# Performance work log

Hardware: AMD Instinct MI355X
Metric: run time of the kernel (lower is better)

The kernel has to match this reference:

```python
import jax, jax.numpy as jnp
from jax import lax
import numpy as np

# Module hyperparameters (match init_kwargs)
N = 4            # number of multiplex cells per feature map
NUM_FM = 64      # feature maps in the input
NF = N * NUM_FM  # lateral channel count = 256
H = W = 32       # feature map height/width
D = 2            # lateral neighborhood radius
PRD = 2          # padding repair distance (must equal D for symmetric pad)
KS = 2 * D + 1   # lateral kernel size = 5
IOTA = 0.1       # blend of activation vs lateral support for winner selection
B = 16           # batch size


def minmax_fm(x):
    """Min-max normalize each feature map (over the last two dims) to [0,1].
    Degenerate (constant) maps map to 0."""
    mn = jnp.min(x, axis=(-2, -1), keepdims=True)
    mx = jnp.max(x, axis=(-2, -1), keepdims=True)
    denom = mx - mn
    safe = jnp.where(denom > 0, denom, 1.0)
    return jnp.where(denom > 0, (x - mn) / safe, 0.0)


def _pad(A):
    # pad_activations: zeros of shape (.., PRD+D+H, PRD+D+W), A at [PRD:-PRD]
    # with PRD == D this is symmetric (PRD, D) padding.
    return jnp.pad(A, ((0, 0), (0, 0), (PRD, D), (PRD, D)))


def _conv(x, w):
    # x: (B, Cin, H', W'), w: (Cout, Cin, KS, KS) -> VALID conv (padding=0)
    return lax.conv_general_dilated(x, w, (1, 1), 'VALID',
                                    dimension_numbers=('NCHW', 'OIHW', 'NCHW'))


def setup_inputs() -> dict:
    key = jax.random.key(0)
    k1, k2 = jax.random.split(key)
    A = jax.random.uniform(k1, (B, NUM_FM, H, W), dtype=jnp.float32)
    K = jax.random.normal(k2, (NF, NF, KS, KS), dtype=jnp.float32)  # trained lateral kernel
    S = jnp.ones((NF,), dtype=jnp.float32)                          # scaling param
    return {"A": A, "K": K, "S": S}


def reference(A, K, S):
    batch = A.shape[0]
    # A.repeat(1, n, 1, 1): tile input n times along channels -> (B, NF, H, W)
    A_rep = jnp.tile(A, (1, N, 1, 1))

    # First lateral pass: conv with minmax-normalized K^T, scaled by S, minmaxed.
    L1 = _conv(_pad(A_rep), minmax_fm(jnp.swapaxes(K, 0, 1))) / NUM_FM
    L1 = L1 * S[None, :, None, None]
    L1 = minmax_fm(L1)

    # Winner-take-all multiplex selection (deterministic branch):
    s = jnp.sum((1.0 - IOTA) * A_rep + IOTA * L1, axis=(-2, -1))  # (B, NF)
    s = jnp.swapaxes(s.reshape(batch, N, NUM_FM), 1, 2)            # (B, NUM_FM, N)
    A_max = jnp.argmax(s, axis=-1)                                  # (B, NUM_FM)
    fm_idx = NUM_FM * A_max + jnp.arange(NUM_FM)                    # (B, NUM_FM) channel ids

    # Active-channel mask (complement = inactive_multiplex_idx in the original)
    active = jnp.zeros((batch, NF), dtype=bool)
    active = active.at[jnp.arange(batch)[:, None], fm_idx].set(True)

    # Zero inactive channels of A (tmp_A) and diagonal K[i,i] for inactive i
    # (large_K[b, idx, idx] = 0 is pairwise/diagonal fancy indexing in torch).
    tmp_A = A_rep * active[:, :, None, None].astype(A_rep.dtype)
    eye = jnp.eye(NF, dtype=bool)
    kill = eye[None, :, :] & (~active)[:, :, None]                  # (B, NF, NF)
    large_K = jnp.where(kill[..., None, None], 0.0, K[None])        # (B, NF, NF, KS, KS)

    # Second lateral pass: per-sample conv with per-sample kernel.
    pA = _pad(tmp_A)

    def per_sample(x, Kb):
        w = minmax_fm(jnp.swapaxes(Kb, 0, 1))
        return _conv(x[None], w)[0]

    L2 = jax.vmap(per_sample)(pA, large_K) / NUM_FM                 # (B, NF, H, W)

    # Gather winning channels: filtered_L (B, NUM_FM, H, W)
    return jnp.take_along_axis(L2, fm_idx[:, :, None, None], axis=1)
```

## Files before the change

kernel.cpp:

```cpp
#include <hip/hip_runtime.h>


#define NFM 64
#define NMX 4
#define NFC 256
#define HW 1024
#define KK 25

typedef unsigned short u16;
typedef short short8 __attribute__((ext_vector_type(8)));
typedef float f32x4 __attribute__((ext_vector_type(4)));

__device__ __forceinline__ u16 f2bfbits(float f) {
    unsigned int u = __float_as_uint(f);
    u += 0x7fffu + ((u >> 16) & 1u);
    return (u16)(u >> 16);
}
__device__ __forceinline__ float bf2f(u16 v) {
    return __uint_as_float(((unsigned int)v) << 16);
}

__global__ __launch_bounds__(256) void kprep(const float* __restrict__ K,
                                             float* __restrict__ wsum2) {
    __shared__ __align__(16) float buf[64 * KK];
    int g = blockIdx.x & 63, o0 = (blockIdx.x >> 6) * 64;
    int t = threadIdx.x;
    float wacc[KK];
#pragma unroll
    for (int k = 0; k < KK; ++k) wacc[k] = 0.f;

    for (int n = 0; n < NMX; ++n) {
        int i = n * NFM + g;
        const float4* src = (const float4*)(K + (i * NFC + o0) * KK);
        __syncthreads();
        ((float4*)buf)[t] = src[t];
        if (t < 144) ((float4*)buf)[t + 256] = src[t + 256];
        __syncthreads();
        if (t < 64) {
            float v[KK];
            float mn = 1e30f, mx = -1e30f;
#pragma unroll
            for (int k = 0; k < KK; ++k) {
                v[k] = buf[t * KK + k];
                mn = fminf(mn, v[k]);
                mx = fmaxf(mx, v[k]);
            }
            float d = mx - mn;
            float r = d > 0.f ? 1.f / d : 0.f;
#pragma unroll
            for (int k = 0; k < KK; ++k) wacc[k] += (v[k] - mn) * r;
        }
    }
    __syncthreads();
    if (t < 64) {
#pragma unroll
        for (int k = 0; k < KK; ++k) buf[t * KK + k] = wacc[k];
    }
    __syncthreads();
    float4* dst = (float4*)(wsum2 + (g * NFC + o0) * KK);
    dst[t] = ((float4*)buf)[t];
    if (t < 144) dst[t + 256] = ((float4*)buf)[t + 256];
}

__global__ __launch_bounds__(256) void kpackW(const float* __restrict__ wsum2,
                                              char* __restrict__ Wpk) {
    int id = blockIdx.x * 256 + threadIdx.x;
    int o = id / 200;
    int rem = id - o * 200;
    int ks = rem >> 2, quad = rem & 3;
    int dydx = ks >> 1;
    int gb = (ks & 1) * 32 + quad * 8;
    short8 hs, ls;
#pragma unroll
    for (int j = 0; j < 8; ++j) {
        float v = wsum2[((gb + j) * NFC + o) * KK + dydx];
        u16 h = f2bfbits(v);
        float lo = v - bf2f(h);
        hs[j] = (short)h;
        ls[j] = (short)f2bfbits(lo);
    }
    char* base = Wpk + (((o >> 4) * 50 + ks) * 2048) + (quad * 16 + (o & 15)) * 16;
    *(short8*)(base) = hs;
    *(short8*)(base + 1024) = ls;
}

__global__ __launch_bounds__(512, 4) void kscore(const float* __restrict__ A,
                                                 const char* __restrict__ Wpk,
                                                 float4* __restrict__ part) {
    __shared__ u16 slabh[6 * 36 * 72];
    __shared__ u16 slabl[6 * 36 * 72];
    int t = threadIdx.x;
    int mh = blockIdx.x, yb2 = blockIdx.y, b = blockIdx.z;
    int y0 = yb2 * 2;
    int lane = t & 63;
    int wv = __builtin_amdgcn_readfirstlane(t >> 6);
    int n15 = lane & 15, quad = lane >> 4;

    const float* Ab = A + b * NFM * HW;
    for (int ry = 0; ry < 6; ++ry) {
        int gy = y0 - 2 + ry;
        bool rowok = (gy >= 0) && (gy < 32);
        for (int c = 0; c < 5; ++c) {
            int id2 = c * 512 + t;
            if (id2 < 2304) {
                int g = (id2 * 3641) >> 17;
                int xi = id2 - g * 36;
                float v = 0.f;
                if (rowok && xi >= 2 && xi < 34)
                    v = Ab[g * HW + gy * 32 + xi - 2];
                u16 h = f2bfbits(v);
                u16 l = f2bfbits(v - bf2f(h));
                int idx = (ry * 36 + xi) * 72 + g;
                slabh[idx] = h;
                slabl[idx] = l;
            }
        }
    }
    __syncthreads();

    f32x4 acc[4];
#pragma unroll
    for (int p = 0; p < 4; ++p)
#pragma unroll
        for (int r = 0; r < 4; ++r) acc[p][r] = 0.f;

    const char* wbase = Wpk + ((mh * 8 + wv) * 50) * 2048 + lane * 16;
    short8 cah = *(const short8*)(wbase);
    short8 cal = *(const short8*)(wbase + 1024);

    for (int ks = 0; ks < 50; ++ks) {
        int ksn = ks < 49 ? ks + 1 : 49;
        const char* nb = wbase + (ksn << 11);
        short8 nah = *(const short8*)nb;
        short8 nal = *(const short8*)(nb + 1024);

        int dydx = ks >> 1;
        int gh = (ks & 1) * 32;
        int dy = dydx / 5, dx = dydx - dy * 5;
        short8 bh[4], bl[4];
#pragma unroll
        for (int p = 0; p < 4; ++p) {
            int r = p >> 1, nt = p & 1;
            int addr = ((r + dy) * 36 + nt * 16 + n15 + dx) * 72 + gh + quad * 8;
            bh[p] = *(const short8*)(slabh + addr);
            bl[p] = *(const short8*)(slabl + addr);
        }
#pragma unroll
        for (int p = 0; p < 4; ++p) {
            acc[p] = __builtin_amdgcn_mfma_f32_16x16x32_bf16(cah, bh[p], acc[p], 0, 0, 0);
            acc[p] = __builtin_amdgcn_mfma_f32_16x16x32_bf16(cah, bl[p], acc[p], 0, 0, 0);
            acc[p] = __builtin_amdgcn_mfma_f32_16x16x32_bf16(cal, bh[p], acc[p], 0, 0, 0);
        }
        cah = nah;
        cal = nal;
    }

#pragma unroll
    for (int reg = 0; reg < 4; ++reg) {
        float v0 = acc[0][reg], v1 = acc[1][reg];
        float v2 = acc[2][reg], v3 = acc[3][reg];
        float mn = fminf(fminf(v0, v1), fminf(v2, v3));
        float mx = fmaxf(fmaxf(v0, v1), fmaxf(v2, v3));
        float sm = (v0 + v1) + (v2 + v3);
#pragma unroll
        for (int msk = 1; msk <= 8; msk <<= 1) {
            mn = fminf(mn, __shfl_xor(mn, msk, 64));
            mx = fmaxf(mx, __shfl_xor(mx, msk, 64));
            sm += __shfl_xor(sm, msk, 64);
        }
        if (n15 == 0) {
            int o = (mh * 8 + wv) * 16 + quad * 4 + reg;
            part[(b * NFC + o) * 16 + yb2] = make_float4(mn, mx, sm, 0.f);
        }
    }
}

__global__ __launch_bounds__(256) void kfin(const float4* __restrict__ part,
                                            const float* __restrict__ S,
                                            int* __restrict__ ig) {
    __shared__ float scl[NFC];
    int b = blockIdx.x, t = threadIdx.x;
    const float4* pp = part + (b * NFC + t) * 16;
    float mn = 1e30f, mx = -1e30f, sm = 0.f;
#pragma unroll
    for (int r = 0; r < 16; ++r) {
        float4 p = pp[r];
        mn = fminf(mn, p.x);
        mx = fmaxf(mx, p.y);
        sm += p.z;
    }
    float s = S[t] * (1.f / 64.f);
    float mnv = (s >= 0.f ? mn : mx) * s;
    float mxv = (s >= 0.f ? mx : mn) * s;
    float smv = sm * s;
    float d = mxv - mnv;
    scl[t] = d > 0.f ? (smv - 1024.f * mnv) / d : 0.f;
    __syncthreads();
    if (t < NFM) {
        float best = scl[t];
        int bi = 0;
#pragma unroll
        for (int n = 1; n < NMX; ++n) {
            float v = scl[n * NFM + t];
            if (v > best) { best = v; bi = n; }
        }
        ig[b * NFM + t] = bi * NFM + t;
    }
}

__global__ __launch_bounds__(256) void kpackO(const float* __restrict__ K,
                                              const int* __restrict__ ig,
                                              char* __restrict__ Wob) {
    __shared__ int igL[NFM];
    __shared__ __align__(16) char cbuf[25 * 2048];
    int ft = blockIdx.x, b = blockIdx.y;
    int t = threadIdx.x;
    if (t < NFM) igL[t] = ig[b * NFM + t];
    __syncthreads();
    int g32 = t & 31, fh = t >> 5;
    int quad = g32 >> 3, j = g32 & 7;
    char* wdst = Wob + b * 409600 + ft * 102400;

    for (int half = 0; half < 2; ++half) {
        int i = igL[half * 32 + g32];
#pragma unroll
        for (int e = 0; e < 2; ++e) {
            int f15 = fh * 2 + e;
            int o = igL[ft * 16 + f15];
            const float* src = K + (i * NFC + o) * KK;
            float v[KK];
            float mn = 1e30f, mx = -1e30f;
#pragma unroll
            for (int k = 0; k < KK; ++k) {
                v[k] = src[k];
                mn = fminf(mn, v[k]);
                mx = fmaxf(mx, v[k]);
            }
            float d = mx - mn;
            float r = d > 0.f ? 1.f / d : 0.f;
            char* base = cbuf + (quad * 16 + f15) * 16 + j * 2;
#pragma unroll
            for (int k = 0; k < KK; ++k) {
                float nv = (v[k] - mn) * r;
                u16 h = f2bfbits(nv);
                u16 l = f2bfbits(nv - bf2f(h));
                *(u16*)(base + k * 2048) = h;
                *(u16*)(base + k * 2048 + 1024) = l;
            }
        }
        __syncthreads();
        for (int idx = t; idx < 3200; idx += 256) {
            int ch = idx >> 7, w = idx & 127;
            *(float4*)(wdst + (ch * 2 + half) * 2048 + w * 16) =
                *(const float4*)(cbuf + ch * 2048 + w * 16);
        }
        __syncthreads();
    }
}

__global__ __launch_bounds__(256, 4) void kout(const float* __restrict__ A,
                                               const char* __restrict__ Wob,
                                               float* __restrict__ out) {
    __shared__ u16 slabh[6 * 20 * 72];
    __shared__ u16 slabl[6 * 20 * 72];
    int t = threadIdx.x;
    int xh = blockIdx.x, yb2 = blockIdx.y, b = blockIdx.z;
    int y0 = yb2 * 2, x0 = xh * 16;
    int lane = t & 63;
    int wv = __builtin_amdgcn_readfirstlane(t >> 6);
    int n15 = lane & 15, quad = lane >> 4;

    const float* Ab = A + b * NFM * HW;
    for (int ry = 0; ry < 6; ++ry) {
        int gy = y0 - 2 + ry;
        bool rowok = (gy >= 0) && (gy < 32);
        for (int c = 0; c < 5; ++c) {
            int id2 = c * 256 + t;
            int g = (id2 * 6554) >> 17;
            int xi = id2 - g * 20;
            int x = x0 + xi - 2;
            float v = 0.f;
            if (rowok && x >= 0 && x < 32)
                v = Ab[g * HW + gy * 32 + x];
            u16 h = f2bfbits(v);
            u16 l = f2bfbits(v - bf2f(h));
            int idx = (ry * 20 + xi) * 72 + g;
            slabh[idx] = h;
            slabl[idx] = l;
        }
    }
    __syncthreads();

    f32x4 acc[2];
#pragma unroll
    for (int r = 0; r < 2; ++r)
#pragma unroll
        for (int jr = 0; jr < 4; ++jr) acc[r][jr] = 0.f;

    const char* wbase = Wob + b * 409600 + (wv * 50) * 2048 + lane * 16;
    short8 cah = *(const short8*)(wbase);
    short8 cal = *(const short8*)(wbase + 1024);

    for (int ks = 0; ks < 50; ++ks) {
        int ksn = ks < 49 ? ks + 1 : 49;
        const char* nb = wbase + (ksn << 11);
        short8 nah = *(const short8*)nb;
        short8 nal = *(const short8*)(nb + 1024);

        int dydx = ks >> 1;
        int gh = (ks & 1) * 32;
        int dy = dydx / 5, dx = dydx - dy * 5;
#pragma unroll
        for (int r = 0; r < 2; ++r) {
            int addr = ((r + dy) * 20 + n15 + dx) * 72 + gh + quad * 8;
            short8 bh = *(const short8*)(slabh + addr);
            short8 bl = *(const short8*)(slabl + addr);
            acc[r] = __builtin_amdgcn_mfma_f32_16x16x32_bf16(cah, bh, acc[r], 0, 0, 0);
            acc[r] = __builtin_amdgcn_mfma_f32_16x16x32_bf16(cah, bl, acc[r], 0, 0, 0);
            acc[r] = __builtin_amdgcn_mfma_f32_16x16x32_bf16(cal, bh, acc[r], 0, 0, 0);
        }
        cah = nah;
        cal = nal;
    }

#pragma unroll
    for (int r = 0; r < 2; ++r)
#pragma unroll
        for (int reg = 0; reg < 4; ++reg) {
            int f = wv * 16 + quad * 4 + reg;
            out[(b * NFM + f) * HW + (y0 + r) * 32 + x0 + n15] = acc[r][reg] * (1.f / 64.f);
        }
}

extern "C" void kernel_launch(void* const* d_in, const int* in_sizes, int n_in,
                              void* d_out, int out_size, void* d_ws, size_t ws_size,
                              hipStream_t stream) {
    const float* A = (const float*)d_in[0];
    const float* K = (const float*)d_in[1];
    const float* S = (const float*)d_in[2];
    float* out = (float*)d_out;

    char* ws = (char*)d_ws;
    char*   Wpk   = ws;
    float*  wsum2 = (float*)(ws + 1638400);
    float4* part  = (float4*)(ws + 3276800);
    char*   Wob   = ws + 1638400;
    int*    igv   = (int*)(ws + 8192000);

    kprep<<<dim3(256), dim3(256), 0, stream>>>(K, wsum2);
    kpackW<<<dim3(200), dim3(256), 0, stream>>>(wsum2, Wpk);
    kscore<<<dim3(2, 16, 16), dim3(512), 0, stream>>>(A, Wpk, part);
    kfin<<<dim3(16), dim3(256), 0, stream>>>(part, S, igv);
    kpackO<<<dim3(4, 16), dim3(256), 0, stream>>>(K, igv, Wob);
    kout<<<dim3(2, 16, 16), dim3(256), 0, stream>>>(A, Wob, out);
}
```

Measured before the change: 154.8 us.

## Retile score kernel to one row per block covering all channels per wave

kscore now uses one output row per block, and each wave computes two 16-channel output tiles, so every activation fragment loaded from LDS feeds two sets of MFMAs. The slab shrinks to 5 rows and the grid becomes 32x16 blocks. wsum2 is transposed to [g][k][o] so that kpackW can stage it through LDS with coalesced loads. Partial statistics are stored as float triples over 32 rows, and workspace offsets are rearranged so that Wob aliases Wpk. The trade-off is twice as many weight reads per wave and twice as many partials for kfin to reduce.

```diff
diff --git a/kernel.cpp b/kernel.cpp
--- a/kernel.cpp
+++ b/kernel.cpp
@@ -57,48 +57,52 @@
         for (int k = 0; k < KK; ++k) buf[t * KK + k] = wacc[k];
     }
     __syncthreads();
-    float4* dst = (float4*)(wsum2 + (g * NFC + o0) * KK);
-    dst[t] = ((float4*)buf)[t];
-    if (t < 144) dst[t + 256] = ((float4*)buf)[t + 256];
+    for (int idx = t; idx < 1600; idx += 256) {
+        int k = idx >> 6, ol = idx & 63;
+        wsum2[(g * KK + k) * NFC + o0 + ol] = buf[ol * KK + k];
+    }
 }
 
 __global__ __launch_bounds__(256) void kpackW(const float* __restrict__ wsum2,
                                               char* __restrict__ Wpk) {
-    int id = blockIdx.x * 256 + threadIdx.x;
-    int o = id / 200;
-    int rem = id - o * 200;
-    int ks = rem >> 2, quad = rem & 3;
-    int dydx = ks >> 1;
-    int gb = (ks & 1) * 32 + quad * 8;
+    __shared__ float wlds[64 * 16];
+    int dydx = blockIdx.x, ot = blockIdx.y, t = threadIdx.x;
+    int o15 = t & 15, gq = t >> 4;
+#pragma unroll
+    for (int e = 0; e < 4; ++e) {
+        int g = e * 16 + gq;
+        wlds[g * 16 + o15] = wsum2[(g * KK + dydx) * NFC + ot * 16 + o15];
+    }
+    __syncthreads();
+    int gh = t >> 7, l = t & 63;
+    int quad = l >> 4, oo = l & 15;
     short8 hs, ls;
 #pragma unroll
     for (int j = 0; j < 8; ++j) {
-        float v = wsum2[((gb + j) * NFC + o) * KK + dydx];
+        float v = wlds[(gh * 32 + quad * 8 + j) * 16 + oo];
         u16 h = f2bfbits(v);
-        float lo = v - bf2f(h);
         hs[j] = (short)h;
-        ls[j] = (short)f2bfbits(lo);
-    }
-    char* base = Wpk + (((o >> 4) * 50 + ks) * 2048) + (quad * 16 + (o & 15)) * 16;
-    *(short8*)(base) = hs;
-    *(short8*)(base + 1024) = ls;
+        ls[j] = (short)f2bfbits(v - bf2f(h));
+    }
+    char* cb = Wpk + (ot * 50 + dydx * 2 + gh) * 2048 + l * 16;
+    *(short8*)cb = hs;
+    *(short8*)(cb + 1024) = ls;
 }
 
 __global__ __launch_bounds__(512, 4) void kscore(const float* __restrict__ A,
                                                  const char* __restrict__ Wpk,
-                                                 float4* __restrict__ part) {
-    __shared__ u16 slabh[6 * 36 * 72];
-    __shared__ u16 slabl[6 * 36 * 72];
+                                                 float* __restrict__ part) {
+    __shared__ u16 slabh[5 * 36 * 72];
+    __shared__ u16 slabl[5 * 36 * 72];
     int t = threadIdx.x;
-    int mh = blockIdx.x, yb2 = blockIdx.y, b = blockIdx.z;
-    int y0 = yb2 * 2;
+    int y = blockIdx.x, b = blockIdx.y;
     int lane = t & 63;
     int wv = __builtin_amdgcn_readfirstlane(t >> 6);
     int n15 = lane & 15, quad = lane >> 4;
 
     const float* Ab = A + b * NFM * HW;
-    for (int ry = 0; ry < 6; ++ry) {
-        int gy = y0 - 2 + ry;
+    for (int ry = 0; ry < 5; ++ry) {
+        int gy = y - 2 + ry;
         bool rowok = (gy >= 0) && (gy < 32);
         for (int c = 0; c < 5; ++c) {
             int id2 = c * 512 + t;
@@ -118,76 +122,87 @@
     }
     __syncthreads();
 
-    f32x4 acc[4];
-#pragma unroll
-    for (int p = 0; p < 4; ++p)
-#pragma unroll
-        for (int r = 0; r < 4; ++r) acc[p][r] = 0.f;
-
-    const char* wbase = Wpk + ((mh * 8 + wv) * 50) * 2048 + lane * 16;
-    short8 cah = *(const short8*)(wbase);
-    short8 cal = *(const short8*)(wbase + 1024);
+    f32x4 acc[2][2];
+#pragma unroll
+    for (int m = 0; m < 2; ++m)
+#pragma unroll
+        for (int p = 0; p < 2; ++p)
+#pragma unroll
+            for (int r = 0; r < 4; ++r) acc[m][p][r] = 0.f;
+
+    const char* wbase0 = Wpk + (wv * 2) * 50 * 2048 + lane * 16;
+    const char* wbase1 = wbase0 + 50 * 2048;
+    short8 cah0 = *(const short8*)(wbase0);
+    short8 cal0 = *(const short8*)(wbase0 + 1024);
+    short8 cah1 = *(const short8*)(wbase1);
+    short8 cal1 = *(const short8*)(wbase1 + 1024);
 
     for (int ks = 0; ks < 50; ++ks) {
         int ksn = ks < 49 ? ks + 1 : 49;
-        const char* nb = wbase + (ksn << 11);
-        short8 nah = *(const short8*)nb;
-        short8 nal = *(const short8*)(nb + 1024);
+        const char* nb0 = wbase0 + (ksn << 11);
+        const char* nb1 = wbase1 + (ksn << 11);
+        short8 nah0 = *(const short8*)nb0;
+        short8 nal0 = *(const short8*)(nb0 + 1024);
+        short8 nah1 = *(const short8*)nb1;
+        short8 nal1 = *(const short8*)(nb1 + 1024);
 
         int dydx = ks >> 1;
         int gh = (ks & 1) * 32;
         int dy = dydx / 5, dx = dydx - dy * 5;
-        short8 bh[4], bl[4];
-#pragma unroll
-        for (int p = 0; p < 4; ++p) {
-            int r = p >> 1, nt = p & 1;
-            int addr = ((r + dy) * 36 + nt * 16 + n15 + dx) * 72 + gh + quad * 8;
+        short8 bh[2], bl[2];
+#pragma unroll
+        for (int p = 0; p < 2; ++p) {
+            int addr = (dy * 36 + p * 16 + n15 + dx) * 72 + gh + quad * 8;
             bh[p] = *(const short8*)(slabh + addr);
             bl[p] = *(const short8*)(slabl + addr);
         }
 #pragma unroll
-        for (int p = 0; p < 4; ++p) {
-            acc[p] = __builtin_amdgcn_mfma_f32_16x16x32_bf16(cah, bh[p], acc[p], 0, 0, 0);
-            acc[p] = __builtin_amdgcn_mfma_f32_16x16x32_bf16(cah, bl[p], acc[p], 0, 0, 0);
-            acc[p] = __builtin_amdgcn_mfma_f32_16x16x32_bf16(cal, bh[p], acc[p], 0, 0, 0);
-        }
-        cah = nah;
-        cal = nal;
-    }
-
-#pragma unroll
-    for (int reg = 0; reg < 4; ++reg) {
-        float v0 = acc[0][reg], v1 = acc[1][reg];
-        float v2 = acc[2][reg], v3 = acc[3][reg];
-        float mn = fminf(fminf(v0, v1), fminf(v2, v3));
-        float mx = fmaxf(fmaxf(v0, v1), fmaxf(v2, v3));
-        float sm = (v0 + v1) + (v2 + v3);
-#pragma unroll
-        for (int msk = 1; msk <= 8; msk <<= 1) {
-            mn = fminf(mn, __shfl_xor(mn, msk, 64));
-            mx = fmaxf(mx, __shfl_xor(mx, msk, 64));
-            sm += __shfl_xor(sm, msk, 64);
-        }
-        if (n15 == 0) {
-            int o = (mh * 8 + wv) * 16 + quad * 4 + reg;
-            part[(b * NFC + o) * 16 + yb2] = make_float4(mn, mx, sm, 0.f);
-        }
-    }
-}
-
-__global__ __launch_bounds__(256) void kfin(const float4* __restrict__ part,
+        for (int p = 0; p < 2; ++p) {
+            acc[0][p] = __builtin_amdgcn_mfma_f32_16x16x32_bf16(cah0, bh[p], acc[0][p], 0, 0, 0);
+            acc[0][p] = __builtin_amdgcn_mfma_f32_16x16x32_bf16(cah0, bl[p], acc[0][p], 0, 0, 0);
+            acc[0][p] = __builtin_amdgcn_mfma_f32_16x16x32_bf16(cal0, bh[p], acc[0][p], 0, 0, 0);
+            acc[1][p] = __builtin_amdgcn_mfma_f32_16x16x32_bf16(cah1, bh[p], acc[1][p], 0, 0, 0);
+            acc[1][p] = __builtin_amdgcn_mfma_f32_16x16x32_bf16(cah1, bl[p], acc[1][p], 0, 0, 0);
+            acc[1][p] = __builtin_amdgcn_mfma_f32_16x16x32_bf16(cal1, bh[p], acc[1][p], 0, 0, 0);
+        }
+        cah0 = nah0; cal0 = nal0; cah1 = nah1; cal1 = nal1;
+    }
+
+#pragma unroll
+    for (int m = 0; m < 2; ++m) {
+#pragma unroll
+        for (int reg = 0; reg < 4; ++reg) {
+            float v0 = acc[m][0][reg], v1 = acc[m][1][reg];
+            float mn = fminf(v0, v1);
+            float mx = fmaxf(v0, v1);
+            float sm = v0 + v1;
+#pragma unroll
+            for (int msk = 1; msk <= 8; msk <<= 1) {
+                mn = fminf(mn, __shfl_xor(mn, msk, 64));
+                mx = fmaxf(mx, __shfl_xor(mx, msk, 64));
+                sm += __shfl_xor(sm, msk, 64);
+            }
+            if (n15 == 0) {
+                int o = (wv * 2 + m) * 16 + quad * 4 + reg;
+                float* pd = part + ((b * NFC + o) * 32 + y) * 3;
+                pd[0] = mn; pd[1] = mx; pd[2] = sm;
+            }
+        }
+    }
+}
+
+__global__ __launch_bounds__(256) void kfin(const float* __restrict__ part,
                                             const float* __restrict__ S,
                                             int* __restrict__ ig) {
     __shared__ float scl[NFC];
     int b = blockIdx.x, t = threadIdx.x;
-    const float4* pp = part + (b * NFC + t) * 16;
+    const float* pp = part + (b * NFC + t) * 96;
     float mn = 1e30f, mx = -1e30f, sm = 0.f;
 #pragma unroll
-    for (int r = 0; r < 16; ++r) {
-        float4 p = pp[r];
-        mn = fminf(mn, p.x);
-        mx = fmaxf(mx, p.y);
-        sm += p.z;
+    for (int r = 0; r < 32; ++r) {
+        mn = fminf(mn, pp[r * 3]);
+        mx = fmaxf(mx, pp[r * 3 + 1]);
+        sm += pp[r * 3 + 2];
     }
     float s = S[t] * (1.f / 64.f);
     float mnv = (s >= 0.f ? mn : mx) * s;
@@ -341,15 +356,15 @@
     float* out = (float*)d_out;
 
     char* ws = (char*)d_ws;
+    char*   Wob   = ws;
     char*   Wpk   = ws;
     float*  wsum2 = (float*)(ws + 1638400);
-    float4* part  = (float4*)(ws + 3276800);
-    char*   Wob   = ws + 1638400;
-    int*    igv   = (int*)(ws + 8192000);
+    float*  part  = (float*)(ws + 6553600);
+    int*    igv   = (int*)(ws + 8126464);
 
     kprep<<<dim3(256), dim3(256), 0, stream>>>(K, wsum2);
-    kpackW<<<dim3(200), dim3(256), 0, stream>>>(wsum2, Wpk);
-    kscore<<<dim3(2, 16, 16), dim3(512), 0, stream>>>(A, Wpk, part);
+    kpackW<<<dim3(25, 16), dim3(256), 0, stream>>>(wsum2, Wpk);
+    kscore<<<dim3(32, 16), dim3(512), 0, stream>>>(A, Wpk, part);
     kfin<<<dim3(16), dim3(256), 0, stream>>>(part, S, igv);
     kpackO<<<dim3(4, 16), dim3(256), 0, stream>>>(K, igv, Wob);
     kout<<<dim3(2, 16, 16), dim3(256), 0, stream>>>(A, Wob, out);
```

Measured after the change: 161.2 us. +4.1%, slower.
